# Kernel optimization log

Hardware: AMD Instinct MI355X
Metric: run time of the kernel (lower is better)

The kernel has to match this reference:

```python
import jax, jax.numpy as jnp
import numpy as np

ALPHA = 0.2  # LeakyReLU negative slope


def setup_inputs() -> dict:
    key = jax.random.key(0)
    k1, k2, k3, k4 = jax.random.split(key, 4)
    n, t, N, c, o = 16, 12, 64, 64, 64
    inp = jax.random.normal(k1, (n, t, N, c), dtype=jnp.float32)
    adj = jax.random.uniform(k2, (t, N, N), dtype=jnp.float32)
    # xavier_uniform with gain=1.414 ~ U(-b, b), b = gain*sqrt(6/(fan_in+fan_out))
    bW = 1.414 * np.sqrt(6.0 / (c + o))
    W = jax.random.uniform(k3, (c, o), dtype=jnp.float32, minval=-bW, maxval=bW)
    ba = 1.414 * np.sqrt(6.0 / (2 * o + 1))
    a = jax.random.uniform(k4, (2 * o, 1), dtype=jnp.float32, minval=-ba, maxval=ba)
    return {"inp": inp, "adj": adj, "W": W, "a": a}


def reference(inp, adj, W, a):
    n, t, N, c = inp.shape
    o = W.shape[1]
    # h: [n,t,N,o]
    h = jnp.einsum('ntvc,co->ntvo', inp, W)
    # Literal translation of the torch repeat/cat(dim=1)/view sequence
    a1 = jnp.tile(h, (1, 1, 1, N)).reshape(n, t, N * N, o)   # row v*N+w -> h[v]
    a2 = jnp.tile(h, (1, 1, N, 1))                            # row v*N+w -> h[w]
    # NOTE: original concatenates along dim=1 (time axis), then row-major views
    # to [n,t,N,N,2o]; we reproduce that exact reshape semantics.
    a_input = jnp.concatenate([a1, a2], axis=1).reshape(n, t, N, N, 2 * o)
    e = jax.nn.leaky_relu(
        jnp.einsum('ntvwo,of->ntvwf', a_input, a), negative_slope=ALPHA
    )[..., 0]                                                  # [n,t,N,N]
    # adj path is dead code in the original: both branches set attention = e
    attention = jax.nn.softmax(e, axis=3)
    # dropout with training=False -> identity
    h_prime = jnp.einsum('ntvw,ntwh->ntvh', attention, h)     # [n,t,N,o]
    return jax.nn.elu(h_prime), attention
```

## Files before the change

### kernel.cpp

```cpp
#include <hip/hip_runtime.h>

#define ALPHA 0.2f

__device__ __forceinline__ float leaky(float x){ return x > 0.f ? x : ALPHA * x; }
__device__ __forceinline__ float elu1 (float x){ return x > 0.f ? x : (__expf(x) - 1.f); }

__global__ __launch_bounds__(256) void gat_fused(
    const float* __restrict__ inp,
    const float* __restrict__ W,
    const float* __restrict__ av,
    float* __restrict__ out)
{
    __shared__ __align__(16) float Ws[64*68];
    __shared__ float X [64*65];
    __shared__ float H [64*65];
    __shared__ float aL[128];
    __shared__ float WaA[64], WaB[64], Wa1[64];
    __shared__ float sArr[2][64];
    __shared__ float S0L[64], S1L[64];
    __shared__ __align__(16) float attL[2][32];
    __shared__ __align__(16) float eluL[2][64];

    const int bid = blockIdx.x;
    const int nI  = bid / 12;
    const int tP  = bid - nI * 12;
    const int tid = threadIdx.x;

    const bool firstHalf = (tP < 6);
    const int tt0 = firstHalf ? 2*tP : 2*tP - 12;
    const int tt1 = tt0 + 1;

    const size_t ownBase = (size_t)(nI*12 + tP) * 4096;

    const float4* W4 = (const float4*)W;
    const float4* X4 = (const float4*)(inp + ownBase);
    for (int i = tid; i < 1024; i += 256) {
        int r = i >> 4, c4 = (i & 15) << 2;
        float4 w = W4[i];
        float* dw = &Ws[r*68 + c4];
        dw[0]=w.x; dw[1]=w.y; dw[2]=w.z; dw[3]=w.w;
        float4 x = X4[i];
        float* dx = &X[r*65 + c4];
        dx[0]=x.x; dx[1]=x.y; dx[2]=x.z; dx[3]=x.w;
    }
    if (tid < 128) aL[tid] = av[tid];
    __syncthreads();

    if (tid < 64) {
        const int c = tid;
        const float* wr = &Ws[c*68];
        float sA = 0.f, sB = 0.f;
        #pragma unroll
        for (int k = 0; k < 64; ++k) { float w = wr[k]; sA += w*aL[k]; sB += w*aL[k+64]; }
        WaA[c] = sA; WaB[c] = sB; Wa1[c] = sA + sB;
    }

    {
        const int v = tid >> 2, tk = tid & 3;
        float acc[16];
        #pragma unroll
        for (int j = 0; j < 16; ++j) acc[j] = 0.f;
        const float* xr = &X[v*65];
        for (int c = 0; c < 64; ++c) {
            const float xv = xr[c];
            const float4* wr4 = (const float4*)&Ws[c*68 + tk*16];
            float4 w0 = wr4[0], w1 = wr4[1], w2 = wr4[2], w3 = wr4[3];
            acc[ 0] += xv*w0.x; acc[ 1] += xv*w0.y; acc[ 2] += xv*w0.z; acc[ 3] += xv*w0.w;
            acc[ 4] += xv*w1.x; acc[ 5] += xv*w1.y; acc[ 6] += xv*w1.z; acc[ 7] += xv*w1.w;
            acc[ 8] += xv*w2.x; acc[ 9] += xv*w2.y; acc[10] += xv*w2.z; acc[11] += xv*w2.w;
            acc[12] += xv*w3.x; acc[13] += xv*w3.y; acc[14] += xv*w3.z; acc[15] += xv*w3.w;
        }
        float* hr = &H[v*65 + tk*16];
        #pragma unroll
        for (int j = 0; j < 16; ++j) hr[j] = acc[j];
    }
    __syncthreads();

    if (tid < 128) {
        const int q = tid >> 6, vv = tid & 63;
        const int ttq = q ? tt1 : tt0;
        const float4* xr = (const float4*)(inp + (size_t)(nI*12 + ttq)*4096 + vv*64);
        const float* wv = firstHalf ? Wa1 : ((vv & 1) ? WaB : WaA);
        float s = 0.f;
        #pragma unroll
        for (int u = 0; u < 16; ++u) {
            float4 x = xr[u];
            s += x.x*wv[4*u] + x.y*wv[4*u+1] + x.z*wv[4*u+2] + x.w*wv[4*u+3];
        }
        sArr[q][vv] = s;
    }
    __syncthreads();

    float* out1 = out + ownBase;
    float* out2 = out + 786432 + ownBase;

    if (firstHalf) {
        if (tid < 64) {
            const int k = tid;
            float s0 = 0.f, s1 = 0.f;
            #pragma unroll
            for (int w = 0; w < 32; ++w) { s0 += H[w*65 + k]; s1 += H[(w+32)*65 + k]; }
            S0L[k] = s0; S1L[k] = s1;
        }
        __syncthreads();
        const int v = tid >> 2, tk = tid & 3;
        const int q = v >> 5, vp = v & 31;
        float A = leaky(sArr[q][2*vp]);
        float B = leaky(sArr[q][2*vp + 1]);
        float m  = fmaxf(A, B);
        float eA = __expf(A - m), eB = __expf(B - m);
        float inv = 1.f / (32.f * (eA + eB));
        float pA = eA * inv, pB = eB * inv;
        float4* o1 = (float4*)(out1 + v*64 + tk*16);
        #pragma unroll
        for (int u = 0; u < 4; ++u) {
            const int k0 = tk*16 + u*4;
            float4 r;
            r.x = elu1(pA*S0L[k0+0] + pB*S1L[k0+0]);
            r.y = elu1(pA*S0L[k0+1] + pB*S1L[k0+1]);
            r.z = elu1(pA*S0L[k0+2] + pB*S1L[k0+2]);
            r.w = elu1(pA*S0L[k0+3] + pB*S1L[k0+3]);
            o1[u] = r;
        }
        const float pv = (tk < 2) ? pA : pB;
        const float4 p4 = make_float4(pv, pv, pv, pv);
        float4* o2 = (float4*)(out2 + v*64 + tk*16);
        #pragma unroll
        for (int u = 0; u < 4; ++u) o2[u] = p4;
    } else {
        if (tid < 64) {
            const int q = tid >> 5, wp = tid & 31;
            float cv = leaky(sArr[q][2*wp] + sArr[q][2*wp + 1]);
            float m = cv;
            #pragma unroll
            for (int mask = 16; mask; mask >>= 1) m = fmaxf(m, __shfl_xor(m, mask));
            float e = __expf(cv - m);
            float s = e;
            #pragma unroll
            for (int mask = 16; mask; mask >>= 1) s += __shfl_xor(s, mask);
            attL[q][wp] = e / (2.f * s);
        }
        __syncthreads();
        if (tid < 128) {
            const int q = tid >> 6, k = tid & 63;
            float acc = 0.f;
            #pragma unroll
            for (int wp = 0; wp < 32; ++wp)
                acc += attL[q][wp] * (H[wp*65 + k] + H[(wp+32)*65 + k]);
            eluL[q][k] = elu1(acc);
        }
        __syncthreads();
        const int v = tid >> 2, tk = tid & 3;
        const int q = v >> 5;
        const float4* s1 = (const float4*)&eluL[q][tk*16];
        float4* o1 = (float4*)(out1 + v*64 + tk*16);
        #pragma unroll
        for (int u = 0; u < 4; ++u) o1[u] = s1[u];
        const float4* s2 = (const float4*)&attL[q][(tk & 1)*16];
        float4* o2 = (float4*)(out2 + v*64 + tk*16);
        #pragma unroll
        for (int u = 0; u < 4; ++u) o2[u] = s2[u];
    }
}

extern "C" void kernel_launch(void* const* d_in, const int* in_sizes, int n_in,
                              void* d_out, int out_size, void* d_ws, size_t ws_size,
                              hipStream_t stream) {
    const float* inp = (const float*)d_in[0];
    const float* W   = (const float*)d_in[2];
    const float* av  = (const float*)d_in[3];
    float* out = (float*)d_out;
    gat_fused<<<dim3(192), dim3(256), 0, stream>>>(inp, W, av, out);
}
```

Baseline: 70.42 us.

## Double block threads, prefetch score inputs and overlap column reductions with scoring

Raises the block size from 256 to 512 threads so each thread computes 8 instead of 16 H outputs and writes 8 outputs. The input rows for the attention scores are prefetched into registers before the shared-memory staging. The column sums (S0/S1) and the pre-summed H rows are now computed by idle threads in the same phase as the score dot products, which removes one barrier. Shared tiles are padded to 68 floats so float4 LDS accesses can be used. In exchange the kernel uses more threads per block and holds 16 float4 registers for the prefetch, and a dead leftover code block remains.

```diff
diff --git a/kernel.cpp b/kernel.cpp
--- a/kernel.cpp
+++ b/kernel.cpp
@@ -5,17 +5,17 @@
 __device__ __forceinline__ float leaky(float x){ return x > 0.f ? x : ALPHA * x; }
 __device__ __forceinline__ float elu1 (float x){ return x > 0.f ? x : (__expf(x) - 1.f); }
 
-__global__ __launch_bounds__(256) void gat_fused(
+__global__ __launch_bounds__(512) void gat_fused(
     const float* __restrict__ inp,
     const float* __restrict__ W,
     const float* __restrict__ av,
     float* __restrict__ out)
 {
     __shared__ __align__(16) float Ws[64*68];
-    __shared__ float X [64*65];
-    __shared__ float H [64*65];
-    __shared__ float aL[128];
-    __shared__ float WaA[64], WaB[64], Wa1[64];
+    __shared__ __align__(16) float X [64*68];
+    __shared__ __align__(16) float H [64*68];
+    __shared__ __align__(16) float aL[128];
+    __shared__ __align__(16) float WaA[64], WaB[64], Wa1[64];
     __shared__ float sArr[2][64];
     __shared__ float S0L[64], S1L[64];
     __shared__ __align__(16) float attL[2][32];
@@ -32,62 +32,92 @@
 
     const size_t ownBase = (size_t)(nI*12 + tP) * 4096;
 
+    float4 rr[16];
+    if (tid < 128) {
+        const int q  = tid >> 6, vvl = tid & 63;
+        const int ttq = q ? tt1 : tt0;
+        const float4* xr = (const float4*)(inp + (size_t)(nI*12 + ttq)*4096 + vvl*64);
+        #pragma unroll
+        for (int u = 0; u < 16; ++u) rr[u] = xr[u];
+    }
+
     const float4* W4 = (const float4*)W;
     const float4* X4 = (const float4*)(inp + ownBase);
-    for (int i = tid; i < 1024; i += 256) {
-        int r = i >> 4, c4 = (i & 15) << 2;
-        float4 w = W4[i];
-        float* dw = &Ws[r*68 + c4];
-        dw[0]=w.x; dw[1]=w.y; dw[2]=w.z; dw[3]=w.w;
-        float4 x = X4[i];
-        float* dx = &X[r*65 + c4];
-        dx[0]=x.x; dx[1]=x.y; dx[2]=x.z; dx[3]=x.w;
+    #pragma unroll
+    for (int i = tid; i < 1024; i += 512) {
+        const int r = i >> 4, c4 = (i & 15) << 2;
+        *(float4*)&Ws[r*68 + c4] = W4[i];
+        *(float4*)&X [r*68 + c4] = X4[i];
     }
     if (tid < 128) aL[tid] = av[tid];
     __syncthreads();
 
     if (tid < 64) {
-        const int c = tid;
-        const float* wr = &Ws[c*68];
+        const float4* wr4 = (const float4*)&Ws[tid*68];
+        const float4* a4  = (const float4*)aL;
         float sA = 0.f, sB = 0.f;
         #pragma unroll
-        for (int k = 0; k < 64; ++k) { float w = wr[k]; sA += w*aL[k]; sB += w*aL[k+64]; }
-        WaA[c] = sA; WaB[c] = sB; Wa1[c] = sA + sB;
+        for (int u = 0; u < 16; ++u) {
+            const float4 w = wr4[u], x = a4[u], y = a4[u+16];
+            sA += w.x*x.x + w.y*x.y + w.z*x.z + w.w*x.w;
+            sB += w.x*y.x + w.y*y.y + w.z*y.z + w.w*y.w;
+        }
+        WaA[tid] = sA; WaB[tid] = sB; Wa1[tid] = sA + sB;
     }
 
     {
-        const int v = tid >> 2, tk = tid & 3;
-        float acc[16];
+        const int v = tid >> 3, tk = tid & 7;
+        float a0=0,a1=0,a2=0,a3=0,a4=0,a5=0,a6=0,a7=0;
+        const float* xr = &X[v*68];
         #pragma unroll
-        for (int j = 0; j < 16; ++j) acc[j] = 0.f;
-        const float* xr = &X[v*65];
         for (int c = 0; c < 64; ++c) {
             const float xv = xr[c];
-            const float4* wr4 = (const float4*)&Ws[c*68 + tk*16];
-            float4 w0 = wr4[0], w1 = wr4[1], w2 = wr4[2], w3 = wr4[3];
-            acc[ 0] += xv*w0.x; acc[ 1] += xv*w0.y; acc[ 2] += xv*w0.z; acc[ 3] += xv*w0.w;
-            acc[ 4] += xv*w1.x; acc[ 5] += xv*w1.y; acc[ 6] += xv*w1.z; acc[ 7] += xv*w1.w;
-            acc[ 8] += xv*w2.x; acc[ 9] += xv*w2.y; acc[10] += xv*w2.z; acc[11] += xv*w2.w;
-            acc[12] += xv*w3.x; acc[13] += xv*w3.y; acc[14] += xv*w3.z; acc[15] += xv*w3.w;
+            const float4* wr4 = (const float4*)&Ws[c*68 + tk*8];
+            const float4 w0 = wr4[0], w1 = wr4[1];
+            a0 += xv*w0.x; a1 += xv*w0.y; a2 += xv*w0.z; a3 += xv*w0.w;
+            a4 += xv*w1.x; a5 += xv*w1.y; a6 += xv*w1.z; a7 += xv*w1.w;
         }
-        float* hr = &H[v*65 + tk*16];
-        #pragma unroll
-        for (int j = 0; j < 16; ++j) hr[j] = acc[j];
+        float* hr = &H[v*68 + tk*8];
+        *(float4*)hr       = make_float4(a0,a1,a2,a3);
+        *(float4*)(hr + 4) = make_float4(a4,a5,a6,a7);
     }
     __syncthreads();
 
     if (tid < 128) {
-        const int q = tid >> 6, vv = tid & 63;
-        const int ttq = q ? tt1 : tt0;
-        const float4* xr = (const float4*)(inp + (size_t)(nI*12 + ttq)*4096 + vv*64);
-        const float* wv = firstHalf ? Wa1 : ((vv & 1) ? WaB : WaA);
+        const int q = tid >> 6, vvl = tid & 63;
+        const float* wv = firstHalf ? Wa1 : ((vvl & 1) ? WaB : WaA);
+        const float4* wv4 = (const float4*)wv;
         float s = 0.f;
         #pragma unroll
         for (int u = 0; u < 16; ++u) {
-            float4 x = xr[u];
-            s += x.x*wv[4*u] + x.y*wv[4*u+1] + x.z*wv[4*u+2] + x.w*wv[4*u+3];
+            const float4 x = rr[u], w = wv4[u];
+            s += x.x*w.x + x.y*w.y + x.z*w.z + x.w*w.w;
         }
-        sArr[q][vv] = s;
+        sArr[q][vvl] = s;
+    } else if (firstHalf) {
+        if (tid < 192) {
+            const int k = tid - 128;
+            float s0 = 0.f, s1 = 0.f;
+            #pragma unroll
+            for (int w = 0; w < 32; ++w) { s0 += H[w*68 + k]; s1 += H[(w+32)*68 + k]; }
+            S0L[k] = s0; S1L[k] = s1;
+        }
+    } else {
+        if (tid < 384) {
+            const int idx = tid - 128;
+            const int wp = idx >> 5, k0 = (idx & 31) << 1;
+        }
+        if (tid < 384) {
+            const int idx = tid - 128;
+            const int wp = idx >> 3, k0 = (idx & 7) * 8;
+            const float4* h0 = (const float4*)&H[wp*68 + k0];
+            const float4* h1 = (const float4*)&H[(wp+32)*68 + k0];
+            float4 u0 = h0[0], u1 = h0[1], v0 = h1[0], v1 = h1[1];
+            float4 r0 = make_float4(u0.x+v0.x, u0.y+v0.y, u0.z+v0.z, u0.w+v0.w);
+            float4 r1 = make_float4(u1.x+v1.x, u1.y+v1.y, u1.z+v1.z, u1.w+v1.w);
+            *(float4*)&X[wp*68 + k0]     = r0;
+            *(float4*)&X[wp*68 + k0 + 4] = r1;
+        }
     }
     __syncthreads();
 
@@ -95,38 +125,30 @@
     float* out2 = out + 786432 + ownBase;
 
     if (firstHalf) {
-        if (tid < 64) {
-            const int k = tid;
-            float s0 = 0.f, s1 = 0.f;
-            #pragma unroll
-            for (int w = 0; w < 32; ++w) { s0 += H[w*65 + k]; s1 += H[(w+32)*65 + k]; }
-            S0L[k] = s0; S1L[k] = s1;
-        }
-        __syncthreads();
-        const int v = tid >> 2, tk = tid & 3;
+        const int v = tid >> 3, tk = tid & 7;
         const int q = v >> 5, vp = v & 31;
-        float A = leaky(sArr[q][2*vp]);
-        float B = leaky(sArr[q][2*vp + 1]);
-        float m  = fmaxf(A, B);
-        float eA = __expf(A - m), eB = __expf(B - m);
-        float inv = 1.f / (32.f * (eA + eB));
-        float pA = eA * inv, pB = eB * inv;
-        float4* o1 = (float4*)(out1 + v*64 + tk*16);
-        #pragma unroll
-        for (int u = 0; u < 4; ++u) {
-            const int k0 = tk*16 + u*4;
-            float4 r;
-            r.x = elu1(pA*S0L[k0+0] + pB*S1L[k0+0]);
-            r.y = elu1(pA*S0L[k0+1] + pB*S1L[k0+1]);
-            r.z = elu1(pA*S0L[k0+2] + pB*S1L[k0+2]);
-            r.w = elu1(pA*S0L[k0+3] + pB*S1L[k0+3]);
-            o1[u] = r;
-        }
-        const float pv = (tk < 2) ? pA : pB;
+        const float A = leaky(sArr[q][2*vp]);
+        const float B = leaky(sArr[q][2*vp + 1]);
+        const float m  = fmaxf(A, B);
+        const float eA = __expf(A - m), eB = __expf(B - m);
+        const float inv = 1.f / (32.f * (eA + eB));
+        const float pA = eA * inv, pB = eB * inv;
+        const int k0 = tk * 8;
+        float4 r0, r1;
+        r0.x = elu1(pA*S0L[k0+0] + pB*S1L[k0+0]);
+        r0.y = elu1(pA*S0L[k0+1] + pB*S1L[k0+1]);
+        r0.z = elu1(pA*S0L[k0+2] + pB*S1L[k0+2]);
+        r0.w = elu1(pA*S0L[k0+3] + pB*S1L[k0+3]);
+        r1.x = elu1(pA*S0L[k0+4] + pB*S1L[k0+4]);
+        r1.y = elu1(pA*S0L[k0+5] + pB*S1L[k0+5]);
+        r1.z = elu1(pA*S0L[k0+6] + pB*S1L[k0+6]);
+        r1.w = elu1(pA*S0L[k0+7] + pB*S1L[k0+7]);
+        float4* o1 = (float4*)(out1 + v*64 + k0);
+        o1[0] = r0; o1[1] = r1;
+        const float pv = (tk < 4) ? pA : pB;
         const float4 p4 = make_float4(pv, pv, pv, pv);
-        float4* o2 = (float4*)(out2 + v*64 + tk*16);
-        #pragma unroll
-        for (int u = 0; u < 4; ++u) o2[u] = p4;
+        float4* o2 = (float4*)(out2 + v*64 + k0);
+        o2[0] = p4; o2[1] = p4;
     } else {
         if (tid < 64) {
             const int q = tid >> 5, wp = tid & 31;
@@ -134,7 +156,7 @@
             float m = cv;
             #pragma unroll
             for (int mask = 16; mask; mask >>= 1) m = fmaxf(m, __shfl_xor(m, mask));
-            float e = __expf(cv - m);
+            const float e = __expf(cv - m);
             float s = e;
             #pragma unroll
             for (int mask = 16; mask; mask >>= 1) s += __shfl_xor(s, mask);
@@ -146,20 +168,19 @@
             float acc = 0.f;
             #pragma unroll
             for (int wp = 0; wp < 32; ++wp)
-                acc += attL[q][wp] * (H[wp*65 + k] + H[(wp+32)*65 + k]);
+                acc += attL[q][wp] * X[wp*68 + k];
             eluL[q][k] = elu1(acc);
         }
         __syncthreads();
-        const int v = tid >> 2, tk = tid & 3;
+        const int v = tid >> 3, tk = tid & 7;
         const int q = v >> 5;
-        const float4* s1 = (const float4*)&eluL[q][tk*16];
-        float4* o1 = (float4*)(out1 + v*64 + tk*16);
-        #pragma unroll
-        for (int u = 0; u < 4; ++u) o1[u] = s1[u];
-        const float4* s2 = (const float4*)&attL[q][(tk & 1)*16];
-        float4* o2 = (float4*)(out2 + v*64 + tk*16);
-        #pragma unroll
-        for (int u = 0; u < 4; ++u) o2[u] = s2[u];
+        const int k0 = tk * 8;
+        const float4* s1 = (const float4*)&eluL[q][k0];
+        float4* o1 = (float4*)(out1 + v*64 + k0);
+        o1[0] = s1[0]; o1[1] = s1[1];
+        const float4* s2 = (const float4*)&attL[q][(tk & 3)*8];
+        float4* o2 = (float4*)(out2 + v*64 + k0);
+        o2[0] = s2[0]; o2[1] = s2[1];
     }
 }
 
@@ -170,5 +191,5 @@
     const float* W   = (const float*)d_in[2];
     const float* av  = (const float*)d_in[3];
     float* out = (float*)d_out;
-    gat_fused<<<dim3(192), dim3(256), 0, stream>>>(inp, W, av, out);
+    gat_fused<<<dim3(192), dim3(512), 0, stream>>>(inp, W, av, out);
 }
```

Result: faster. 66.82 us (-5.1%).
